# Kernel optimization log

Hardware: AMD Instinct MI355X
Metric: run time of the kernel (lower is better)

The kernel has to match this reference:

```python
import jax, jax.numpy as jnp
import numpy as np

E = 1024  # encoding_size
K_STEPS = 8  # processing_steps


def setup_inputs() -> dict:
    key = jax.random.key(0)
    k1, k2, k3, k4, k5, k6 = jax.random.split(key, 6)
    B, T, N, k = 32, 128, 64, 5
    scale = 1.0 / np.sqrt(E)  # torch LSTMCell default init scale
    return {
        "targets": jax.random.normal(k1, (B, T, E), dtype=jnp.float32),
        "support_embeddings": jax.random.normal(k2, (B, N, k, E), dtype=jnp.float32),
        "W_ih": jax.random.normal(k3, (4 * E, E), dtype=jnp.float32) * scale,
        "W_hh": jax.random.normal(k4, (4 * E, E), dtype=jnp.float32) * scale,
        "b_ih": jax.random.normal(k5, (4 * E,), dtype=jnp.float32) * scale,
        "b_hh": jax.random.normal(k6, (4 * E,), dtype=jnp.float32) * scale,
    }


def _lstm_cell(x, h, c, W_ih, W_hh, b_ih, b_hh):
    # torch LSTMCell gate order: i, f, g, o
    gates = x @ W_ih.T + b_ih + h @ W_hh.T + b_hh  # [BT, 4E]
    i, f, g, o = jnp.split(gates, 4, axis=-1)
    i, f, o = jax.nn.sigmoid(i), jax.nn.sigmoid(f), jax.nn.sigmoid(o)
    g = jnp.tanh(g)
    c_next = f * c + i * g
    h_next = o * jnp.tanh(c_next)
    return h_next, c_next


def reference(targets, support_embeddings, W_ih, W_hh, b_ih, b_hh):
    B, T, enc = targets.shape
    N, k = support_embeddings.shape[1], support_embeddings.shape[2]
    x = targets.reshape(-1, enc)  # [B*T, E]
    zeros = jnp.zeros_like(x)

    def step(carry, _):
        h_prev, c_prev, r_prev = carry
        h_prev = h_prev + r_prev  # h_prev += r_prev (read step)
        h_next, c_next = _lstm_cell(x, h_prev, c_prev, W_ih, W_hh, b_ih, b_hh)
        h_next = h_next + x  # skip connection
        # attention over the support set, softmax over flattened (N*k)
        q = h_prev.reshape(B, T, enc)
        dots = jnp.einsum('bte,bnke->btnk', q, support_embeddings)
        att = jax.nn.softmax(dots.reshape(B, T, N * k), axis=2).reshape(B, T, N, k)
        r_next = jnp.einsum('btnk,bnke->bte', att, support_embeddings).reshape(-1, enc)
        return (h_next, c_next, r_next), None

    (h, _, _), _ = jax.lax.scan(step, (zeros, zeros, zeros), None, length=K_STEPS)
    return h.reshape(B, T, enc)
```

## Files before the change

kernel.cpp:

```cpp
#include <hip/hip_runtime.h>
#include <math.h>

#define E_DIM   1024
#define M_ROWS  4096
#define NKP     320
#define GATES_N 4096
#define MF      (M_ROWS * E_DIM)
#define SF      ((size_t)32 * NKP * E_DIM)
#define AST     328

typedef __attribute__((ext_vector_type(8))) short bf16x8;
typedef __attribute__((ext_vector_type(4))) float f32x4;

__device__ float          g_Gx[(size_t)M_ROWS * GATES_N];
__device__ float          g_h[MF], g_c[MF], g_r[MF];
__device__ unsigned short g_hinh[MF], g_hinm[MF], g_hinl[MF];
__device__ unsigned short g_xh[MF],   g_xm[MF];
__device__ unsigned short g_Wihh[MF], g_Wihm[MF];
__device__ unsigned short g_Whhh[MF], g_Whhm[MF];
__device__ unsigned short g_Sh[SF], g_Sm[SF], g_Sl[SF];
__device__ unsigned short g_STh[SF], g_STm[SF];

__device__ __forceinline__ unsigned short f2bf(float f) {
    unsigned int u = __builtin_bit_cast(unsigned int, f);
    return (unsigned short)((u + 0x7fffu + ((u >> 16) & 1u)) >> 16);
}
__device__ __forceinline__ float bf2f(unsigned short s) {
    unsigned int u = ((unsigned int)s) << 16;
    return __builtin_bit_cast(float, u);
}
__device__ __forceinline__ void split2(float v, unsigned short& hi, unsigned short& mi) {
    hi = f2bf(v); mi = f2bf(v - bf2f(hi));
}
__device__ __forceinline__ void split3(float v, unsigned short& hi, unsigned short& mi,
                                       unsigned short& lo) {
    hi = f2bf(v);
    const float r1 = v - bf2f(hi);
    mi = f2bf(r1);
    lo = f2bf(r1 - bf2f(mi));
}
__device__ __forceinline__ float sigmoid_f(float v) { return 1.f / (1.f + __expf(-v)); }
__device__ __forceinline__ float tanh_f(float v) {
    const float vc = fminf(fmaxf(v, -15.f), 15.f);
    const float t = __expf(2.f * vc);
    return (t - 1.f) / (t + 1.f);
}

union SharedU {
    struct { unsigned short A2[2][256 * 64]; unsigned short B2[2][256 * 64]; } g;
    struct {
        unsigned short ah[32][AST], am[32][AST];
        float red_m[4][32], red_s[4][32];
    } a;
};

__global__ __launch_bounds__(256) void prep_kernel(
    const float* __restrict__ Wih, const float* __restrict__ Whh,
    const float* __restrict__ x)
{
    const int i = blockIdx.x * 256 + threadIdx.x;
    const float4 w4 = reinterpret_cast<const float4*>(Wih)[i];
    const float4 v4 = reinterpret_cast<const float4*>(Whh)[i];
    const float4 x4 = reinterpret_cast<const float4*>(x)[i];
    ushort4 ah, am, bh, bm, ch, cm;
    split2(w4.x, ah.x, am.x); split2(w4.y, ah.y, am.y);
    split2(w4.z, ah.z, am.z); split2(w4.w, ah.w, am.w);
    split2(v4.x, bh.x, bm.x); split2(v4.y, bh.y, bm.y);
    split2(v4.z, bh.z, bm.z); split2(v4.w, bh.w, bm.w);
    split2(x4.x, ch.x, cm.x); split2(x4.y, ch.y, cm.y);
    split2(x4.z, ch.z, cm.z); split2(x4.w, ch.w, cm.w);
    reinterpret_cast<ushort4*>(g_Wihh)[i] = ah; reinterpret_cast<ushort4*>(g_Wihm)[i] = am;
    reinterpret_cast<ushort4*>(g_Whhh)[i] = bh; reinterpret_cast<ushort4*>(g_Whhm)[i] = bm;
    reinterpret_cast<ushort4*>(g_xh)[i]   = ch; reinterpret_cast<ushort4*>(g_xm)[i]   = cm;
    const float4 z = make_float4(0.f, 0.f, 0.f, 0.f);
    reinterpret_cast<float4*>(g_h)[i] = z;
    reinterpret_cast<float4*>(g_c)[i] = z;
    reinterpret_cast<float4*>(g_r)[i] = z;
}

__global__ __launch_bounds__(256) void split_S_kernel(const float* __restrict__ S)
{
    __shared__ float t[64][65];
    const int b = blockIdx.z, j0 = blockIdx.y * 64, k0 = blockIdx.x * 64;
    const float* Sb = S + (size_t)b * NKP * E_DIM;
    const int c = threadIdx.x & 63, r4 = threadIdx.x >> 6;
    #pragma unroll
    for (int i = 0; i < 16; ++i) {
        const int row = r4 * 16 + i;
        const float v = Sb[(size_t)(j0 + row) * E_DIM + k0 + c];
        t[row][c] = v;
        unsigned short hi, mi, lo;
        split3(v, hi, mi, lo);
        const size_t si = (size_t)b * NKP * E_DIM + (size_t)(j0 + row) * E_DIM + k0 + c;
        g_Sh[si] = hi; g_Sm[si] = mi; g_Sl[si] = lo;
    }
    __syncthreads();
    #pragma unroll
    for (int i = 0; i < 16; ++i) {
        const int row = r4 * 16 + i;
        const float v = t[c][row];
        unsigned short hi, mi;
        split2(v, hi, mi);
        const size_t sti = (size_t)b * E_DIM * NKP + (size_t)(k0 + row) * NKP + j0 + c;
        g_STh[sti] = hi; g_STm[sti] = mi;
    }
}

__global__ __launch_bounds__(256) void add_split3_kernel()
{
    const int i = blockIdx.x * 256 + threadIdx.x;
    const float4 a = reinterpret_cast<const float4*>(g_h)[i];
    const float4 b = reinterpret_cast<const float4*>(g_r)[i];
    ushort4 oh, om, ol;
    split3(a.x + b.x, oh.x, om.x, ol.x);
    split3(a.y + b.y, oh.y, om.y, ol.y);
    split3(a.z + b.z, oh.z, om.z, ol.z);
    split3(a.w + b.w, oh.w, om.w, ol.w);
    reinterpret_cast<ushort4*>(g_hinh)[i] = oh;
    reinterpret_cast<ushort4*>(g_hinm)[i] = om;
    reinterpret_cast<ushort4*>(g_hinl)[i] = ol;
}

__global__ __launch_bounds__(256, 2) void gemm_gx_kernel(
    const float* __restrict__ bih, const float* __restrict__ bhh)
{
    __shared__ struct { unsigned short A2[2][128 * 64]; unsigned short B2[2][128 * 64]; } sh;
    const int tid = threadIdx.x, l = tid & 63, w = tid >> 6;
    const int b15 = l & 15, lg = l >> 4, x7 = b15 & 7;
    const int d = blockIdx.x;
    const int j = d >> 3;
    const int row0 = (j >> 2) * 128, e0 = ((d & 7) * 4 + (j & 3)) * 32;
    const int arow = w * 32 + b15;
    f32x4 acc[2][8] = {};

    auto stage = [&](int bf, int kt) {
        #pragma unroll
        for (int it = 0; it < 4; ++it) {
            const int slot = it * 256 + tid;
            const int row  = slot >> 3;
            const int chs  = (slot & 7) ^ (row & 7);
            const int kb   = (chs & 3) * 8;
            const unsigned short* sA = (chs & 4) ? g_xm   : g_xh;
            const unsigned short* sB = (chs & 4) ? g_Wihm : g_Wihh;
            const int ldsoff = bf * 16384 + slot * 16;
            const size_t aidx = (size_t)(row0 + row) * E_DIM + kt + kb;
            const int gt = row >> 5, er = row & 31;
            const size_t bidx = (size_t)(gt * E_DIM + e0 + er) * E_DIM + kt + kb;
            __builtin_amdgcn_global_load_lds(
                (const __attribute__((address_space(1))) void*)&sA[aidx],
                (__attribute__((address_space(3))) void*)((char*)sh.A2 + ldsoff), 16, 0, 0);
            __builtin_amdgcn_global_load_lds(
                (const __attribute__((address_space(1))) void*)&sB[bidx],
                (__attribute__((address_space(3))) void*)((char*)sh.B2 + ldsoff), 16, 0, 0);
        }
    };

    stage(0, 0);
    int cur = 0;
    for (int kt = 0; kt < E_DIM; kt += 32) {
        if (kt + 32 < E_DIM) {
            stage(cur ^ 1, kt + 32);
            asm volatile("s_waitcnt vmcnt(8)" ::: "memory");
        } else {
            asm volatile("s_waitcnt vmcnt(0)" ::: "memory");
        }
        __builtin_amdgcn_sched_barrier(0);
        __builtin_amdgcn_s_barrier();
        __builtin_amdgcn_sched_barrier(0);
        const unsigned short* Ab = sh.A2[cur];
        const unsigned short* Bb = sh.B2[cur];
        bf16x8 avh[2], avm[2];
        #pragma unroll
        for (int m = 0; m < 2; ++m) {
            const int rr = arow + m * 16;
            avh[m] = *reinterpret_cast<const bf16x8*>(&Ab[rr * 64 + ((lg ^ x7) * 8)]);
            avm[m] = *reinterpret_cast<const bf16x8*>(&Ab[rr * 64 + (((4 | lg) ^ x7) * 8)]);
        }
        #pragma unroll
        for (int n = 0; n < 8; ++n) {
            const int br = n * 16 + b15;
            const bf16x8 bvh = *reinterpret_cast<const bf16x8*>(&Bb[br * 64 + ((lg ^ x7) * 8)]);
            const bf16x8 bvm = *reinterpret_cast<const bf16x8*>(&Bb[br * 64 + (((4 | lg) ^ x7) * 8)]);
            #pragma unroll
            for (int m = 0; m < 2; ++m) {
                acc[m][n] = __builtin_amdgcn_mfma_f32_16x16x32_bf16(avh[m], bvm, acc[m][n], 0, 0, 0);
                acc[m][n] = __builtin_amdgcn_mfma_f32_16x16x32_bf16(avm[m], bvh, acc[m][n], 0, 0, 0);
                acc[m][n] = __builtin_amdgcn_mfma_f32_16x16x32_bf16(avh[m], bvh, acc[m][n], 0, 0, 0);
            }
        }
        __builtin_amdgcn_sched_barrier(0);
        __builtin_amdgcn_s_barrier();
        __builtin_amdgcn_sched_barrier(0);
        cur ^= 1;
    }

    const int rbase = row0 + w * 32 + lg * 4;
    #pragma unroll
    for (int m = 0; m < 2; ++m)
        #pragma unroll
        for (int n = 0; n < 8; ++n) {
            const int col = n * 16 + b15;
            const int gcol = (col >> 5) * E_DIM + e0 + (col & 31);
            const float add = bih[gcol] + bhh[gcol];
            #pragma unroll
            for (int q = 0; q < 4; ++q)
                __builtin_nontemporal_store(acc[m][n][q] + add,
                    &g_Gx[(size_t)(rbase + m * 16 + q) * GATES_N + gcol]);
        }
}

__global__ __launch_bounds__(512, 2) void step_kernel(
    const float* __restrict__ x, float* __restrict__ outp, const int step)
{
    __shared__ SharedU sh;
    const int tid = threadIdx.x, l = tid & 63, w = tid >> 6;
    const int b15 = l & 15, lg = l >> 4, x7 = b15 & 7;

    if (blockIdx.x < 128) {
        if (step == 7) return;
        const int d = blockIdx.x;
        const int i = d >> 3;
        const int batch = (d & 7) * 4 + (i >> 2), chunk = i & 3;
        const int rowbase = batch * 128 + chunk * 32;
        const size_t sbase  = (size_t)batch * NKP * E_DIM;
        const size_t stbase = (size_t)batch * E_DIM * NKP;
        const int mq = w >> 2, ws = w & 3;

        f32x4 qacc[5] = {};
        for (int kt = 0; kt < E_DIM; kt += 32) {
            const size_t qi = (size_t)(rowbase + mq * 16 + b15) * E_DIM + kt + lg * 8;
            const bf16x8 qh = *reinterpret_cast<const bf16x8*>(&g_hinh[qi]);
            const bf16x8 qm = *reinterpret_cast<const bf16x8*>(&g_hinm[qi]);
            const bf16x8 ql = *reinterpret_cast<const bf16x8*>(&g_hinl[qi]);
            #pragma unroll
            for (int n = 0; n < 5; ++n) {
                const size_t si = sbase + (size_t)(ws * 80 + n * 16 + b15) * E_DIM + kt + lg * 8;
                const bf16x8 svh = *reinterpret_cast<const bf16x8*>(&g_Sh[si]);
                const bf16x8 svm = *reinterpret_cast<const bf16x8*>(&g_Sm[si]);
                const bf16x8 svl = *reinterpret_cast<const bf16x8*>(&g_Sl[si]);
                f32x4 a = qacc[n];
                a = __builtin_amdgcn_mfma_f32_16x16x32_bf16(qh, svl, a, 0, 0, 0);
                a = __builtin_amdgcn_mfma_f32_16x16x32_bf16(ql, svh, a, 0, 0, 0);
                a = __builtin_amdgcn_mfma_f32_16x16x32_bf16(qm, svm, a, 0, 0, 0);
                a = __builtin_amdgcn_mfma_f32_16x16x32_bf16(qh, svm, a, 0, 0, 0);
                a = __builtin_amdgcn_mfma_f32_16x16x32_bf16(qm, svh, a, 0, 0, 0);
                a = __builtin_amdgcn_mfma_f32_16x16x32_bf16(qh, svh, a, 0, 0, 0);
                qacc[n] = a;
            }
        }

        #pragma unroll
        for (int q = 0; q < 4; ++q) {
            float m0 = qacc[0][q];
            #pragma unroll
            for (int n = 1; n < 5; ++n) m0 = fmaxf(m0, qacc[n][q]);
            #pragma unroll
            for (int mk = 1; mk < 16; mk <<= 1) m0 = fmaxf(m0, __shfl_xor(m0, mk));
            if (b15 == 0) sh.a.red_m[ws][mq * 16 + lg * 4 + q] = m0;
        }
        __syncthreads();
        #pragma unroll
        for (int q = 0; q < 4; ++q) {
            const int row = mq * 16 + lg * 4 + q;
            const float gm = fmaxf(fmaxf(sh.a.red_m[0][row], sh.a.red_m[1][row]),
                                   fmaxf(sh.a.red_m[2][row], sh.a.red_m[3][row]));
            float s = 0.f;
            #pragma unroll
            for (int n = 0; n < 5; ++n) {
                const float e = __expf(qacc[n][q] - gm);
                qacc[n][q] = e;
                s += e;
            }
            #pragma unroll
            for (int mk = 1; mk < 16; mk <<= 1) s += __shfl_xor(s, mk);
            if (b15 == 0) sh.a.red_s[ws][row] = s;
        }
        __syncthreads();
        #pragma unroll
        for (int q = 0; q < 4; ++q) {
            const int row = mq * 16 + lg * 4 + q;
            const float inv = 1.f / (sh.a.red_s[0][row] + sh.a.red_s[1][row] +
                                     sh.a.red_s[2][row] + sh.a.red_s[3][row]);
            #pragma unroll
            for (int n = 0; n < 5; ++n) {
                const float a = qacc[n][q] * inv;
                unsigned short hi, mi;
                split2(a, hi, mi);
                const int col = ws * 80 + n * 16 + b15;
                sh.a.ah[row][col] = hi;
                sh.a.am[row][col] = mi;
            }
        }
        __syncthreads();

        #pragma unroll 1
        for (int pass = 0; pass < 2; ++pass) {
            const int ebase = w * 128 + pass * 64;
            f32x4 pacc[2][4] = {};
            for (int jt = 0; jt < NKP; jt += 32) {
                bf16x8 pah[2], pam[2];
                #pragma unroll
                for (int m = 0; m < 2; ++m) {
                    pah[m] = *reinterpret_cast<const bf16x8*>(&sh.a.ah[m * 16 + b15][jt + lg * 8]);
                    pam[m] = *reinterpret_cast<const bf16x8*>(&sh.a.am[m * 16 + b15][jt + lg * 8]);
                }
                #pragma unroll
                for (int n = 0; n < 4; ++n) {
                    const size_t sti = stbase + (size_t)(ebase + n * 16 + b15) * NKP + jt + lg * 8;
                    const bf16x8 sth = *reinterpret_cast<const bf16x8*>(&g_STh[sti]);
                    const bf16x8 stm = *reinterpret_cast<const bf16x8*>(&g_STm[sti]);
                    #pragma unroll
                    for (int m = 0; m < 2; ++m) {
                        f32x4 a = pacc[m][n];
                        a = __builtin_amdgcn_mfma_f32_16x16x32_bf16(pah[m], stm, a, 0, 0, 0);
                        a = __builtin_amdgcn_mfma_f32_16x16x32_bf16(pam[m], sth, a, 0, 0, 0);
                        a = __builtin_amdgcn_mfma_f32_16x16x32_bf16(pah[m], sth, a, 0, 0, 0);
                        pacc[m][n] = a;
                    }
                }
            }
            #pragma unroll
            for (int m = 0; m < 2; ++m)
                #pragma unroll
                for (int n = 0; n < 4; ++n)
                    #pragma unroll
                    for (int q = 0; q < 4; ++q)
                        __builtin_nontemporal_store(pacc[m][n][q],
                            &g_r[(size_t)(rowbase + m * 16 + lg * 4 + q) * E_DIM +
                                 ebase + n * 16 + b15]);
        }
        return;
    }

    const int d2 = blockIdx.x - 128;
    const int idx = d2 >> 3;
    const int row0 = (idx & 15) * 256;
    const int e0   = ((d2 & 7) * 2 + (idx >> 4)) * 64;
    const int wm = w >> 2, wn = w & 3;
    f32x4 acc[8][4] = {};

    auto stage = [&](int bf, int kt) {
        #pragma unroll
        for (int it = 0; it < 4; ++it) {
            const int slot = it * 512 + tid;
            const int row  = slot >> 3;
            const int chs  = (slot & 7) ^ (row & 7);
            const int kb   = (chs & 3) * 8;
            const unsigned short* sA = (chs & 4) ? g_hinm : g_hinh;
            const int ldsoff = bf * 32768 + slot * 16;
            const size_t aidx = (size_t)(row0 + row) * E_DIM + kt + kb;
            __builtin_amdgcn_global_load_lds(
                (const __attribute__((address_space(1))) void*)&sA[aidx],
                (__attribute__((address_space(3))) void*)((char*)sh.g.A2 + ldsoff), 16, 0, 0);
        }
        #pragma unroll
        for (int it = 0; it < 4; ++it) {
            const int slot = it * 512 + tid;
            const int row  = slot >> 3;
            const int chs  = (slot & 7) ^ (row & 7);
            const int kb   = (chs & 3) * 8;
            const unsigned short* sB = (chs & 4) ? g_Whhm : g_Whhh;
            const int ldsoff = bf * 32768 + slot * 16;
            const int gt = row >> 6, er = row & 63;
            const size_t bidx = (size_t)(gt * E_DIM + e0 + er) * E_DIM + kt + kb;
            __builtin_amdgcn_global_load_lds(
                (const __attribute__((address_space(1))) void*)&sB[bidx],
                (__attribute__((address_space(3))) void*)((char*)sh.g.B2 + ldsoff), 16, 0, 0);
        }
    };

    stage(0, 0);
    int cur = 0;
    for (int kt = 0; kt < E_DIM; kt += 32) {
        if (kt + 32 < E_DIM) {
            stage(cur ^ 1, kt + 32);
            asm volatile("s_waitcnt vmcnt(8)" ::: "memory");
        } else {
            asm volatile("s_waitcnt vmcnt(0)" ::: "memory");
        }
        __builtin_amdgcn_sched_barrier(0);
        __builtin_amdgcn_s_barrier();
        __builtin_amdgcn_sched_barrier(0);
        const unsigned short* Ab = sh.g.A2[cur];
        const unsigned short* Bb = sh.g.B2[cur];
        bf16x8 bvh[4], bvm[4];
        #pragma unroll
        for (int n = 0; n < 4; ++n) {
            const int rb = n * 64 + wn * 16 + b15;
            bvh[n] = *reinterpret_cast<const bf16x8*>(&Bb[rb * 64 + ((lg ^ x7) * 8)]);
            bvm[n] = *reinterpret_cast<const bf16x8*>(&Bb[rb * 64 + (((4 | lg) ^ x7) * 8)]);
        }
        #pragma unroll
        for (int mg = 0; mg < 2; ++mg) {
            bf16x8 avh[4], avm[4];
            #pragma unroll
            for (int mi = 0; mi < 4; ++mi) {
                const int ra = wm * 128 + (mg * 4 + mi) * 16 + b15;
                avh[mi] = *reinterpret_cast<const bf16x8*>(&Ab[ra * 64 + ((lg ^ x7) * 8)]);
                avm[mi] = *reinterpret_cast<const bf16x8*>(&Ab[ra * 64 + (((4 | lg) ^ x7) * 8)]);
            }
            #pragma unroll
            for (int mi = 0; mi < 4; ++mi)
                #pragma unroll
                for (int n = 0; n < 4; ++n) {
                    const int m = mg * 4 + mi;
                    acc[m][n] = __builtin_amdgcn_mfma_f32_16x16x32_bf16(avh[mi], bvm[n], acc[m][n], 0, 0, 0);
                    acc[m][n] = __builtin_amdgcn_mfma_f32_16x16x32_bf16(avm[mi], bvh[n], acc[m][n], 0, 0, 0);
                    acc[m][n] = __builtin_amdgcn_mfma_f32_16x16x32_bf16(avh[mi], bvh[n], acc[m][n], 0, 0, 0);
                }
        }
        __builtin_amdgcn_sched_barrier(0);
        __builtin_amdgcn_s_barrier();
        __builtin_amdgcn_sched_barrier(0);
        cur ^= 1;
    }

    const int e = e0 + wn * 16 + b15;
    const int do_out = (step == 7);
    #pragma unroll
    for (int m = 0; m < 8; ++m) {
        const int rbase = row0 + wm * 128 + m * 16 + lg * 4;
        #pragma unroll
        for (int q = 0; q < 4; ++q) {
            const int row = rbase + q;
            const size_t gb = (size_t)row * GATES_N + e;
            const float gi = acc[m][0][q] + __builtin_nontemporal_load(&g_Gx[gb]);
            const float gf = acc[m][1][q] + __builtin_nontemporal_load(&g_Gx[gb + E_DIM]);
            const float gg = acc[m][2][q] + __builtin_nontemporal_load(&g_Gx[gb + 2 * E_DIM]);
            const float go = acc[m][3][q] + __builtin_nontemporal_load(&g_Gx[gb + 3 * E_DIM]);
            const size_t he = (size_t)row * E_DIM + e;
            const float cn = sigmoid_f(gf) * __builtin_nontemporal_load(&g_c[he]) +
                             sigmoid_f(gi) * tanh_f(gg);
            __builtin_nontemporal_store(cn, &g_c[he]);
            const float hn = sigmoid_f(go) * tanh_f(cn) + x[he];
            g_h[he] = hn;
            if (do_out) __builtin_nontemporal_store(hn, &outp[he]);
        }
    }
}

extern "C" void kernel_launch(void* const* d_in, const int* in_sizes, int n_in,
                              void* d_out, int out_size, void* d_ws, size_t ws_size,
                              hipStream_t stream) {
    const float* x   = (const float*)d_in[0];
    const float* sup = (const float*)d_in[1];
    const float* Wih = (const float*)d_in[2];
    const float* Whh = (const float*)d_in[3];
    const float* bih = (const float*)d_in[4];
    const float* bhh = (const float*)d_in[5];
    float* out = (float*)d_out;

    prep_kernel<<<4096, 256, 0, stream>>>(Wih, Whh, x);
    split_S_kernel<<<dim3(16, 5, 32), 256, 0, stream>>>(sup);
    gemm_gx_kernel<<<1024, 256, 0, stream>>>(bih, bhh);

    for (int s = 0; s < 8; ++s) {
        add_split3_kernel<<<4096, 256, 0, stream>>>();
        step_kernel<<<384, 512, 0, stream>>>(x, out, s);
    }
}
```

Measured before the change: 2.260 ms.

## Specialize first LSTM step analytically and retile recurrent GEMM with triple buffering

Step 0 is computed in closed form: h and c start at zero, so the recurrent GEMM is skipped, the gates come from Gx alone, and the initial attention over zero queries reduces to the mean of the support set. A new meanS kernel precomputes that mean and a fused step0 kernel writes c and the split h+r. The per-step GEMM tile is halved to 128 rows (640 blocks) and now uses a 3-stage LDS pipeline with s_setprio around the MFMAs. Launch order is reshuffled so the step kernel runs before add_split3, which drops one step kernel plus one elementwise pass. The catch is that correctness depends on the step kernel's attention branch also producing r for the next step.

New measurement: 2.019 ms. 10.7% less time.

```diff
diff --git a/kernel.cpp b/kernel.cpp
--- a/kernel.cpp
+++ b/kernel.cpp
@@ -14,6 +14,7 @@
 
 __device__ float          g_Gx[(size_t)M_ROWS * GATES_N];
 __device__ float          g_h[MF], g_c[MF], g_r[MF];
+__device__ float          g_meanS[32 * E_DIM];
 __device__ unsigned short g_hinh[MF], g_hinm[MF], g_hinl[MF];
 __device__ unsigned short g_xh[MF],   g_xm[MF];
 __device__ unsigned short g_Wihh[MF], g_Wihm[MF];
@@ -47,7 +48,7 @@
 }
 
 union SharedU {
-    struct { unsigned short A2[2][256 * 64]; unsigned short B2[2][256 * 64]; } g;
+    struct { unsigned short A2[3][128 * 64]; unsigned short B2[3][256 * 64]; } g;
     struct {
         unsigned short ah[32][AST], am[32][AST];
         float red_m[4][32], red_s[4][32];
@@ -104,6 +105,50 @@
         const size_t sti = (size_t)b * E_DIM * NKP + (size_t)(k0 + row) * NKP + j0 + c;
         g_STh[sti] = hi; g_STm[sti] = mi;
     }
+}
+
+__global__ __launch_bounds__(256) void meanS_kernel(const float* __restrict__ S)
+{
+    const int b = blockIdx.x >> 2;
+    const int e = (blockIdx.x & 3) * 256 + threadIdx.x;
+    const float* Sb = S + (size_t)b * NKP * E_DIM + e;
+    float s = 0.f;
+    #pragma unroll 4
+    for (int j = 0; j < NKP; ++j) s += Sb[(size_t)j * E_DIM];
+    g_meanS[b * E_DIM + e] = s * (1.0f / NKP);
+}
+
+__global__ __launch_bounds__(256) void step0_kernel(const float* __restrict__ x)
+{
+    const int i = blockIdx.x * 256 + threadIdx.x;
+    const int row = i >> 8, col4 = i & 255;
+    const int b = row >> 7;
+    const float4 m4 = reinterpret_cast<const float4*>(g_meanS)[b * 256 + col4];
+    const float4 x4 = reinterpret_cast<const float4*>(x)[i];
+    const float4 gi4 = reinterpret_cast<const float4*>(g_Gx)[row * 1024 + col4];
+    const float4 gg4 = reinterpret_cast<const float4*>(g_Gx)[row * 1024 + 512 + col4];
+    const float4 go4 = reinterpret_cast<const float4*>(g_Gx)[row * 1024 + 768 + col4];
+    float4 c4, hin4;
+    {
+        const float c0 = sigmoid_f(gi4.x) * tanh_f(gg4.x);
+        const float c1 = sigmoid_f(gi4.y) * tanh_f(gg4.y);
+        const float c2 = sigmoid_f(gi4.z) * tanh_f(gg4.z);
+        const float c3 = sigmoid_f(gi4.w) * tanh_f(gg4.w);
+        c4 = make_float4(c0, c1, c2, c3);
+        hin4.x = sigmoid_f(go4.x) * tanh_f(c0) + x4.x + m4.x;
+        hin4.y = sigmoid_f(go4.y) * tanh_f(c1) + x4.y + m4.y;
+        hin4.z = sigmoid_f(go4.z) * tanh_f(c2) + x4.z + m4.z;
+        hin4.w = sigmoid_f(go4.w) * tanh_f(c3) + x4.w + m4.w;
+    }
+    reinterpret_cast<float4*>(g_c)[i] = c4;
+    ushort4 oh, om, ol;
+    split3(hin4.x, oh.x, om.x, ol.x);
+    split3(hin4.y, oh.y, om.y, ol.y);
+    split3(hin4.z, oh.z, om.z, ol.z);
+    split3(hin4.w, oh.w, om.w, ol.w);
+    reinterpret_cast<ushort4*>(g_hinh)[i] = oh;
+    reinterpret_cast<ushort4*>(g_hinm)[i] = om;
+    reinterpret_cast<ushort4*>(g_hinl)[i] = ol;
 }
 
 __global__ __launch_bounds__(256) void add_split3_kernel()
@@ -334,24 +379,24 @@
 
     const int d2 = blockIdx.x - 128;
     const int idx = d2 >> 3;
-    const int row0 = (idx & 15) * 256;
-    const int e0   = ((d2 & 7) * 2 + (idx >> 4)) * 64;
+    const int row0 = (idx & 31) * 128;
+    const int e0   = ((d2 & 7) * 2 + (idx >> 5)) * 64;
     const int wm = w >> 2, wn = w & 3;
-    f32x4 acc[8][4] = {};
+    f32x4 acc[4][4] = {};
 
     auto stage = [&](int bf, int kt) {
         #pragma unroll
-        for (int it = 0; it < 4; ++it) {
+        for (int it = 0; it < 2; ++it) {
             const int slot = it * 512 + tid;
             const int row  = slot >> 3;
             const int chs  = (slot & 7) ^ (row & 7);
             const int kb   = (chs & 3) * 8;
             const unsigned short* sA = (chs & 4) ? g_hinm : g_hinh;
-            const int ldsoff = bf * 32768 + slot * 16;
             const size_t aidx = (size_t)(row0 + row) * E_DIM + kt + kb;
             __builtin_amdgcn_global_load_lds(
                 (const __attribute__((address_space(1))) void*)&sA[aidx],
-                (__attribute__((address_space(3))) void*)((char*)sh.g.A2 + ldsoff), 16, 0, 0);
+                (__attribute__((address_space(3))) void*)((char*)sh.g.A2[bf] + slot * 16),
+                16, 0, 0);
         }
         #pragma unroll
         for (int it = 0; it < 4; ++it) {
@@ -360,74 +405,72 @@
             const int chs  = (slot & 7) ^ (row & 7);
             const int kb   = (chs & 3) * 8;
             const unsigned short* sB = (chs & 4) ? g_Whhm : g_Whhh;
-            const int ldsoff = bf * 32768 + slot * 16;
             const int gt = row >> 6, er = row & 63;
             const size_t bidx = (size_t)(gt * E_DIM + e0 + er) * E_DIM + kt + kb;
             __builtin_amdgcn_global_load_lds(
                 (const __attribute__((address_space(1))) void*)&sB[bidx],
-                (__attribute__((address_space(3))) void*)((char*)sh.g.B2 + ldsoff), 16, 0, 0);
+                (__attribute__((address_space(3))) void*)((char*)sh.g.B2[bf] + slot * 16),
+                16, 0, 0);
         }
     };
 
     stage(0, 0);
-    int cur = 0;
-    for (int kt = 0; kt < E_DIM; kt += 32) {
-        if (kt + 32 < E_DIM) {
-            stage(cur ^ 1, kt + 32);
-            asm volatile("s_waitcnt vmcnt(8)" ::: "memory");
+    stage(1, 32);
+    for (int k = 0; k < 32; ++k) {
+        if (k < 31) {
+            asm volatile("s_waitcnt vmcnt(6)" ::: "memory");
         } else {
             asm volatile("s_waitcnt vmcnt(0)" ::: "memory");
         }
         __builtin_amdgcn_sched_barrier(0);
         __builtin_amdgcn_s_barrier();
         __builtin_amdgcn_sched_barrier(0);
-        const unsigned short* Ab = sh.g.A2[cur];
-        const unsigned short* Bb = sh.g.B2[cur];
+        const int bf = k % 3;
+        if (k + 2 < 32) stage((k + 2) % 3, (k + 2) * 32);
+        const unsigned short* Ab = sh.g.A2[bf];
+        const unsigned short* Bb = sh.g.B2[bf];
         bf16x8 bvh[4], bvm[4];
         #pragma unroll
-        for (int n = 0; n < 4; ++n) {
-            const int rb = n * 64 + wn * 16 + b15;
-            bvh[n] = *reinterpret_cast<const bf16x8*>(&Bb[rb * 64 + ((lg ^ x7) * 8)]);
-            bvm[n] = *reinterpret_cast<const bf16x8*>(&Bb[rb * 64 + (((4 | lg) ^ x7) * 8)]);
-        }
-        #pragma unroll
-        for (int mg = 0; mg < 2; ++mg) {
-            bf16x8 avh[4], avm[4];
-            #pragma unroll
-            for (int mi = 0; mi < 4; ++mi) {
-                const int ra = wm * 128 + (mg * 4 + mi) * 16 + b15;
-                avh[mi] = *reinterpret_cast<const bf16x8*>(&Ab[ra * 64 + ((lg ^ x7) * 8)]);
-                avm[mi] = *reinterpret_cast<const bf16x8*>(&Ab[ra * 64 + (((4 | lg) ^ x7) * 8)]);
+        for (int g = 0; g < 4; ++g) {
+            const int rb = g * 64 + wn * 16 + b15;
+            bvh[g] = *reinterpret_cast<const bf16x8*>(&Bb[rb * 64 + ((lg ^ x7) * 8)]);
+            bvm[g] = *reinterpret_cast<const bf16x8*>(&Bb[rb * 64 + (((4 | lg) ^ x7) * 8)]);
+        }
+        bf16x8 avh[4], avm[4];
+        #pragma unroll
+        for (int mi = 0; mi < 4; ++mi) {
+            const int ra = wm * 64 + mi * 16 + b15;
+            avh[mi] = *reinterpret_cast<const bf16x8*>(&Ab[ra * 64 + ((lg ^ x7) * 8)]);
+            avm[mi] = *reinterpret_cast<const bf16x8*>(&Ab[ra * 64 + (((4 | lg) ^ x7) * 8)]);
+        }
+        __builtin_amdgcn_s_setprio(1);
+        #pragma unroll
+        for (int mi = 0; mi < 4; ++mi)
+            #pragma unroll
+            for (int g = 0; g < 4; ++g) {
+                acc[mi][g] = __builtin_amdgcn_mfma_f32_16x16x32_bf16(avh[mi], bvm[g], acc[mi][g], 0, 0, 0);
+                acc[mi][g] = __builtin_amdgcn_mfma_f32_16x16x32_bf16(avm[mi], bvh[g], acc[mi][g], 0, 0, 0);
+                acc[mi][g] = __builtin_amdgcn_mfma_f32_16x16x32_bf16(avh[mi], bvh[g], acc[mi][g], 0, 0, 0);
             }
-            #pragma unroll
-            for (int mi = 0; mi < 4; ++mi)
-                #pragma unroll
-                for (int n = 0; n < 4; ++n) {
-                    const int m = mg * 4 + mi;
-                    acc[m][n] = __builtin_amdgcn_mfma_f32_16x16x32_bf16(avh[mi], bvm[n], acc[m][n], 0, 0, 0);
-                    acc[m][n] = __builtin_amdgcn_mfma_f32_16x16x32_bf16(avm[mi], bvh[n], acc[m][n], 0, 0, 0);
-                    acc[m][n] = __builtin_amdgcn_mfma_f32_16x16x32_bf16(avh[mi], bvh[n], acc[m][n], 0, 0, 0);
-                }
-        }
+        __builtin_amdgcn_s_setprio(0);
         __builtin_amdgcn_sched_barrier(0);
         __builtin_amdgcn_s_barrier();
         __builtin_amdgcn_sched_barrier(0);
-        cur ^= 1;
     }
 
     const int e = e0 + wn * 16 + b15;
     const int do_out = (step == 7);
     #pragma unroll
-    for (int m = 0; m < 8; ++m) {
-        const int rbase = row0 + wm * 128 + m * 16 + lg * 4;
+    for (int mi = 0; mi < 4; ++mi) {
+        const int rbase = row0 + wm * 64 + mi * 16 + lg * 4;
         #pragma unroll
         for (int q = 0; q < 4; ++q) {
             const int row = rbase + q;
             const size_t gb = (size_t)row * GATES_N + e;
-            const float gi = acc[m][0][q] + __builtin_nontemporal_load(&g_Gx[gb]);
-            const float gf = acc[m][1][q] + __builtin_nontemporal_load(&g_Gx[gb + E_DIM]);
-            const float gg = acc[m][2][q] + __builtin_nontemporal_load(&g_Gx[gb + 2 * E_DIM]);
-            const float go = acc[m][3][q] + __builtin_nontemporal_load(&g_Gx[gb + 3 * E_DIM]);
+            const float gi = acc[mi][0][q] + __builtin_nontemporal_load(&g_Gx[gb]);
+            const float gf = acc[mi][1][q] + __builtin_nontemporal_load(&g_Gx[gb + E_DIM]);
+            const float gg = acc[mi][2][q] + __builtin_nontemporal_load(&g_Gx[gb + 2 * E_DIM]);
+            const float go = acc[mi][3][q] + __builtin_nontemporal_load(&g_Gx[gb + 3 * E_DIM]);
             const size_t he = (size_t)row * E_DIM + e;
             const float cn = sigmoid_f(gf) * __builtin_nontemporal_load(&g_c[he]) +
                              sigmoid_f(gi) * tanh_f(gg);
@@ -453,9 +496,12 @@
     prep_kernel<<<4096, 256, 0, stream>>>(Wih, Whh, x);
     split_S_kernel<<<dim3(16, 5, 32), 256, 0, stream>>>(sup);
     gemm_gx_kernel<<<1024, 256, 0, stream>>>(bih, bhh);
-
-    for (int s = 0; s < 8; ++s) {
-        add_split3_kernel<<<4096, 256, 0, stream>>>();
-        step_kernel<<<384, 512, 0, stream>>>(x, out, s);
-    }
-}
+    meanS_kernel<<<128, 256, 0, stream>>>(sup);
+
+    step0_kernel<<<4096, 256, 0, stream>>>(x);
+
+    for (int s = 1; s < 8; ++s) {
+        step_kernel<<<640, 512, 0, stream>>>(x, out, s);
+        if (s < 7) add_split3_kernel<<<4096, 256, 0, stream>>>();
+    }
+}
```
